# Kernel optimization log

Hardware: AMD Instinct MI355X
Metric: run time of the kernel (lower is better)

The kernel has to match this reference:

```python
import jax, jax.numpy as jnp
import numpy as np

N_NODES = 163840
N_EDGES = 2621440
F_IN = 64
F_HID = 64
SUBG = 20  # size_subgraph_samples
NEG_SLOPE = 0.2


def gat_conv(x, src, dst, W, a_src, a_dst, b):
    """PyG GATConv, heads=1, concat. src/dst already include self-loops."""
    n = x.shape[0]
    h = x @ W                               # [N, H]
    al_s = h @ a_src                        # [N]
    al_d = h @ a_dst                        # [N]
    e = jax.nn.leaky_relu(al_s[src] + al_d[dst], NEG_SLOPE)  # [E]
    # softmax over incoming edges of each dst node
    m = jax.ops.segment_max(e, dst, num_segments=n)
    ex = jnp.exp(e - m[dst])
    denom = jax.ops.segment_sum(ex, dst, num_segments=n)
    alpha = ex / (denom[dst] + 1e-16)
    msg = h[src] * alpha[:, None]           # [E, H]
    out = jax.ops.segment_sum(msg, dst, num_segments=n)
    return out + b


def setup_inputs() -> dict:
    key = jax.random.key(0)
    ks = jax.random.split(key, 12)
    s = 0.05
    return {
        "x": jax.random.normal(ks[0], (N_NODES, F_IN), jnp.float32),
        "edge_index": jax.random.randint(ks[1], (2, N_EDGES), 0, N_NODES, jnp.int64 if jax.config.jax_enable_x64 else jnp.int32),
        "W1": jax.random.normal(ks[2], (F_IN, F_HID), jnp.float32) * s,
        "a_src1": jax.random.normal(ks[3], (F_HID,), jnp.float32) * s,
        "a_dst1": jax.random.normal(ks[4], (F_HID,), jnp.float32) * s,
        "b1": jnp.zeros((F_HID,), jnp.float32),
        "W2": jax.random.normal(ks[5], (F_HID, F_HID), jnp.float32) * s,
        "a_src2": jax.random.normal(ks[6], (F_HID,), jnp.float32) * s,
        "a_dst2": jax.random.normal(ks[7], (F_HID,), jnp.float32) * s,
        "b2": jnp.zeros((F_HID,), jnp.float32),
        "W_out": jax.random.normal(ks[8], (F_HID * SUBG, 1), jnp.float32) * s,
        "b_out": jnp.zeros((1,), jnp.float32),
    }


def reference(x, edge_index, W1, a_src1, a_dst1, b1, W2, a_src2, a_dst2, b2, W_out, b_out):
    n = x.shape[0]
    loop = jnp.arange(n, dtype=edge_index.dtype)
    src = jnp.concatenate([edge_index[0], loop])  # add_self_loops=True
    dst = jnp.concatenate([edge_index[1], loop])
    h = gat_conv(x, src, dst, W1, a_src1, a_dst1, b1)
    h = jax.nn.relu(h)  # dropout is identity in eval mode
    h = gat_conv(h, src, dst, W2, a_src2, a_dst2, b2)
    h = jax.nn.relu(h)
    h = h.reshape(n // SUBG, F_HID * SUBG)
    return h @ W_out + b_out
```

## Files before the change

### kernel.cpp

```cpp
#include <hip/hip_runtime.h>
#include <math.h>

#define F 64
#define NPB 160
#define STAGE_CAP 6304

typedef __attribute__((ext_vector_type(8))) short bf16x8;
typedef __attribute__((ext_vector_type(4))) float f32x4;

__device__ inline unsigned short f2bf(float f) {
  unsigned int u = __float_as_uint(f);
  u += 0x7fffu + ((u >> 16) & 1u);
  return (unsigned short)(u >> 16);
}


__global__ __launch_bounds__(256) void k_bin_count(const int* __restrict__ edst, int* __restrict__ cntT,
                                                   int e, int ch, int nblk, int nb,
                                                   const float* __restrict__ W1, const float* __restrict__ W2,
                                                   uint4* __restrict__ wf) {
  __shared__ int h[1024];
  int k = blockIdx.x, tid = threadIdx.x;
  if (k == nblk) {
    for (int i = tid; i < 1024; i += 256) {
      int layer = i >> 9, rem = i & 511;
      int cb = rem >> 6, lane = rem & 63;
      int c = cb >> 1, kk = cb & 1;
      int l15 = lane & 15, quad = lane >> 4;
      const float* W = layer ? W2 : W1;
      unsigned short p[8];
      #pragma unroll
      for (int j = 0; j < 8; j++) {
        int kd = kk * 32 + quad * 8 + j;
        p[j] = f2bf(W[kd * F + c * 16 + l15]);
      }
      wf[i] = *(const uint4*)p;
    }
    return;
  }
  for (int i = tid; i < nb; i += 256) h[i] = 0;
  __syncthreads();
  int beg = k * ch, end = min(e, beg + ch);
  for (int i = beg + tid; i < end; i += 256) atomicAdd(&h[edst[i] / NPB], 1);
  __syncthreads();
  for (int b = tid; b < nb; b += 256) cntT[b * nblk + k] = h[b];
}

__global__ __launch_bounds__(256) void k_scan1(const int* __restrict__ counts, int* __restrict__ offs,
                                               int* __restrict__ bsums, int n) {
  int tid = threadIdx.x, lane = tid & 63, wv = tid >> 6;
  int i = blockIdx.x * 256 + tid;
  int v = (i < n) ? counts[i] : 0;
  int x = v;
  #pragma unroll
  for (int o = 1; o <= 32; o <<= 1) { int y = __shfl_up(x, o); if (lane >= o) x += y; }
  __shared__ int wsum[4];
  if (lane == 63) wsum[wv] = x;
  __syncthreads();
  int add = 0;
  for (int w = 0; w < wv; w++) add += wsum[w];
  int incl = x + add;
  if (i < n) offs[i] = incl - v;
  if (tid == 255) bsums[blockIdx.x] = incl;
}

__global__ __launch_bounds__(256) void k_scan2(int* __restrict__ bs, int nb,
                                               float* __restrict__ out, const float* __restrict__ bo, int ng) {
  __shared__ int wsum[4];
  __shared__ int carry_sh;
  int tid = threadIdx.x, lane = tid & 63, wv = tid >> 6;
  float b0 = bo[0];
  for (int i = tid; i < ng; i += 256) out[i] = b0;
  if (tid == 0) carry_sh = 0;
  __syncthreads();
  for (int base = 0; base < nb; base += 256) {
    int i = base + tid;
    int v = (i < nb) ? bs[i] : 0;
    int x = v;
    #pragma unroll
    for (int o = 1; o <= 32; o <<= 1) { int y = __shfl_up(x, o); if (lane >= o) x += y; }
    if (lane == 63) wsum[wv] = x;
    __syncthreads();
    int add = 0;
    for (int w = 0; w < wv; w++) add += wsum[w];
    int incl = x + add;
    int carry = carry_sh;
    if (i < nb) bs[i] = incl - v + carry;
    __syncthreads();
    if (tid == 255) carry_sh = carry + incl;
    __syncthreads();
  }
}

template<bool IN_BF16>
__device__ __forceinline__ void gemm_body(const void* __restrict__ in, const uint4* __restrict__ wf,
                                          const float* __restrict__ avs, const float* __restrict__ avd,
                                          unsigned short* __restrict__ hgb, float* __restrict__ als,
                                          float* __restrict__ ald, int n, int bid, int nbl) {
  int tid = threadIdx.x, lane = tid & 63, wv = tid >> 6;
  int l15 = lane & 15, quad = lane >> 4;
  bf16x8 bfr[4][2];
  #pragma unroll
  for (int cb = 0; cb < 8; cb++) {
    uint4 u = wf[cb * 64 + lane];
    bfr[cb >> 1][cb & 1] = *(const bf16x8*)&u;
  }
  float as_l[4], ad_l[4];
  #pragma unroll
  for (int c = 0; c < 4; c++) { as_l[c] = avs[c * 16 + l15]; ad_l[c] = avd[c * 16 + l15]; }

  int nchunks = n >> 6;
  for (int chunk = bid; chunk < nchunks; chunk += nbl) {
    int r0 = (chunk << 6) + (wv << 4);
    bf16x8 a0, a1;
    if constexpr (IN_BF16) {
      const uint4* row4 = (const uint4*)((const unsigned short*)in + (size_t)(r0 + l15) * F);
      uint4 u0 = row4[quad];
      uint4 u1 = row4[quad + 4];
      a0 = *(const bf16x8*)&u0;
      a1 = *(const bf16x8*)&u1;
    } else {
      const float4* xr = (const float4*)((const float*)in + (size_t)(r0 + l15) * F + quad * 8);
      float4 xa = xr[0], xb = xr[1];
      float4 xc = xr[8], xd = xr[9];
      a0[0] = (short)f2bf(xa.x); a0[1] = (short)f2bf(xa.y); a0[2] = (short)f2bf(xa.z); a0[3] = (short)f2bf(xa.w);
      a0[4] = (short)f2bf(xb.x); a0[5] = (short)f2bf(xb.y); a0[6] = (short)f2bf(xb.z); a0[7] = (short)f2bf(xb.w);
      a1[0] = (short)f2bf(xc.x); a1[1] = (short)f2bf(xc.y); a1[2] = (short)f2bf(xc.z); a1[3] = (short)f2bf(xc.w);
      a1[4] = (short)f2bf(xd.x); a1[5] = (short)f2bf(xd.y); a1[6] = (short)f2bf(xd.z); a1[7] = (short)f2bf(xd.w);
    }
    f32x4 cfr[4];
    #pragma unroll
    for (int c = 0; c < 4; c++) {
      cfr[c] = (f32x4){0.f, 0.f, 0.f, 0.f};
      cfr[c] = __builtin_amdgcn_mfma_f32_16x16x32_bf16(a0, bfr[c][0], cfr[c], 0, 0, 0);
      cfr[c] = __builtin_amdgcn_mfma_f32_16x16x32_bf16(a1, bfr[c][1], cfr[c], 0, 0, 0);
    }
    #pragma unroll
    for (int i = 0; i < 4; i++) {
      int row = r0 + quad * 4 + i;
      #pragma unroll
      for (int c = 0; c < 4; c++) hgb[(size_t)row * F + c * 16 + l15] = f2bf(cfr[c][i]);
      float ps = cfr[0][i] * as_l[0] + cfr[1][i] * as_l[1] + cfr[2][i] * as_l[2] + cfr[3][i] * as_l[3];
      float pd = cfr[0][i] * ad_l[0] + cfr[1][i] * ad_l[1] + cfr[2][i] * ad_l[2] + cfr[3][i] * ad_l[3];
      #pragma unroll
      for (int o = 1; o <= 8; o <<= 1) { ps += __shfl_xor(ps, o); pd += __shfl_xor(pd, o); }
      if (l15 == 0) { als[row] = ps; ald[row] = pd; }
    }
  }
}

__global__ __launch_bounds__(256) void k_scatter_gemm1(const int* __restrict__ esrc, const int* __restrict__ edst,
                                                       const int* __restrict__ posT, const int* __restrict__ bsums,
                                                       unsigned int* __restrict__ binned,
                                                       int e, int ch, int nblk, int nb,
                                                       const float* __restrict__ x, const uint4* __restrict__ wf,
                                                       const float* __restrict__ avs, const float* __restrict__ avd,
                                                       unsigned short* __restrict__ hgb, float* __restrict__ als,
                                                       float* __restrict__ ald, int n) {
  int k = blockIdx.x, tid = threadIdx.x;
  if (k < nblk) {
    __shared__ int cur[1024];
    for (int b = tid; b < nb; b += 256) {
      int idx = b * nblk + k;
      cur[b] = posT[idx] + bsums[idx >> 8];
    }
    __syncthreads();
    int beg = k * ch, end = min(e, beg + ch);
    for (int i = beg + tid; i < end; i += 256) {
      int d = edst[i];
      int b = d / NPB;
      unsigned int ld = (unsigned int)(d - b * NPB);
      int p = atomicAdd(&cur[b], 1);
      binned[p] = (unsigned int)esrc[i] | (ld << 24);
    }
    return;
  }
  gemm_body<false>(x, wf, avs, avd, hgb, als, ald, n, k - nblk, (int)gridDim.x - nblk);
}

__global__ __launch_bounds__(256) void k_gemm2(const unsigned short* __restrict__ in, const uint4* __restrict__ wf,
                                               const float* __restrict__ avs, const float* __restrict__ avd,
                                               unsigned short* __restrict__ hgb, float* __restrict__ als,
                                               float* __restrict__ ald, int n) {
  gemm_body<true>(in, wf, avs, avd, hgb, als, ald, n, blockIdx.x, gridDim.x);
}

__global__ __launch_bounds__(256) void k_bucket_csr(const unsigned int* __restrict__ binned,
                                                    const int* __restrict__ posT, const int* __restrict__ bsums,
                                                    int* __restrict__ ssrc, int* __restrict__ offs,
                                                    int n, int nblk, int nb, int e) {
  __shared__ int ncnt[NPB];
  __shared__ int noff[NPB];
  __shared__ int cur[NPB];
  __shared__ int sc[256];
  __shared__ int stage[STAGE_CAP];
  int b = blockIdx.x, tid = threadIdx.x;
  int node0 = b * NPB;
  int nn = min(NPB, n - node0);
  int i0 = b * nblk;
  int ebeg = posT[i0] + bsums[i0 >> 8];
  int eend;
  if (b == nb - 1) eend = e;
  else { int i1 = (b + 1) * nblk; eend = posT[i1] + bsums[i1 >> 8]; }
  int ecnt = eend - ebeg;
  for (int i = tid; i < NPB; i += 256) ncnt[i] = 0;
  __syncthreads();
  for (int i = tid; i < ecnt; i += 256) { unsigned int v = binned[ebeg + i]; atomicAdd(&ncnt[v >> 24], 1); }
  __syncthreads();
  int x = (tid < nn) ? ncnt[tid] + 1 : 0;
  sc[tid] = x;
  __syncthreads();
  #pragma unroll
  for (int o = 1; o < 256; o <<= 1) {
    int y = (tid >= o) ? sc[tid - o] : 0;
    __syncthreads();
    sc[tid] += y;
    __syncthreads();
  }
  if (tid < nn) noff[tid] = sc[tid] - x;
  __syncthreads();
  int tot = ecnt + nn;
  int outbase = ebeg + node0;
  bool staged = (tot <= STAGE_CAP);
  if (tid < nn) {
    cur[tid] = noff[tid] + 1;
    offs[node0 + tid] = outbase + noff[tid];
    if (staged) stage[noff[tid]] = node0 + tid;
    else        ssrc[outbase + noff[tid]] = node0 + tid;
  }
  __syncthreads();
  if (staged) {
    for (int i = tid; i < ecnt; i += 256) {
      unsigned int v = binned[ebeg + i];
      int p = atomicAdd(&cur[v >> 24], 1);
      stage[p] = (int)(v & 0xFFFFFFu);
    }
    __syncthreads();
    for (int i = tid; i < tot; i += 256) ssrc[outbase + i] = stage[i];
  } else {
    for (int i = tid; i < ecnt; i += 256) {
      unsigned int v = binned[ebeg + i];
      int p = atomicAdd(&cur[v >> 24], 1);
      ssrc[outbase + p] = (int)(v & 0xFFFFFFu);
    }
  }
  if (b == 0 && tid == 0) offs[n] = e + n;
}

template<int MODE>
__global__ __launch_bounds__(256) void k_spmm(const int* __restrict__ offs, const int* __restrict__ ssrc,
                                              const unsigned short* __restrict__ hgb,
                                              const float* __restrict__ als, const float* __restrict__ ald,
                                              const float* __restrict__ bias, const float* __restrict__ Wout,
                                              void* __restrict__ outp, int n) {
  int tid = threadIdx.x, lane = tid & 63, wv = tid >> 6;
  int g8 = lane >> 3, l8 = lane & 7;
  const uint4* hg4 = (const uint4*)hgb;
  float4 bl0 = ((const float4*)bias)[l8 * 2];
  float4 bl1 = ((const float4*)bias)[l8 * 2 + 1];

  __shared__ float gsl[3];
  if (MODE == 1 && tid < 3) gsl[tid] = 0.f;

  int node = (blockIdx.x * 4 + wv) * 8 + g8;
  int cnode = min(node, n - 1);
  bool nodeok = node < n;
  int beg = offs[cnode];
  int deg = nodeok ? (offs[cnode + 1] - beg) : 0;
  int degc = max(deg - 1, 0);
  float aldv = ald[cnode];

  int dm = deg;
  #pragma unroll
  for (int o = 8; o <= 32; o <<= 1) dm = max(dm, __shfl_xor(dm, o));

  float s = 0.f;
  float acc[8];
  #pragma unroll
  for (int k = 0; k < 8; k++) acc[k] = 0.f;

  #pragma unroll 2
  for (int j = 0; j < dm; j++) {
    int jj = min(j, degc);
    int src = ssrc[beg + jj];
    float t = als[src] + aldv;
    t = fmaxf(t, 0.2f * t);
    float ex = (j < deg) ? __expf(t) : 0.f;
    s += ex;
    uint4 u = hg4[(size_t)src * 8 + l8];
    acc[0] = fmaf(ex, __uint_as_float(u.x << 16), acc[0]);
    acc[1] = fmaf(ex, __uint_as_float(u.x & 0xffff0000u), acc[1]);
    acc[2] = fmaf(ex, __uint_as_float(u.y << 16), acc[2]);
    acc[3] = fmaf(ex, __uint_as_float(u.y & 0xffff0000u), acc[3]);
    acc[4] = fmaf(ex, __uint_as_float(u.z << 16), acc[4]);
    acc[5] = fmaf(ex, __uint_as_float(u.z & 0xffff0000u), acc[5]);
    acc[6] = fmaf(ex, __uint_as_float(u.w << 16), acc[6]);
    acc[7] = fmaf(ex, __uint_as_float(u.w & 0xffff0000u), acc[7]);
  }

  float iv = 1.f / (s + 1e-16f);
  float r[8];
  r[0] = fmaxf(fmaf(acc[0], iv, bl0.x), 0.f);
  r[1] = fmaxf(fmaf(acc[1], iv, bl0.y), 0.f);
  r[2] = fmaxf(fmaf(acc[2], iv, bl0.z), 0.f);
  r[3] = fmaxf(fmaf(acc[3], iv, bl0.w), 0.f);
  r[4] = fmaxf(fmaf(acc[4], iv, bl1.x), 0.f);
  r[5] = fmaxf(fmaf(acc[5], iv, bl1.y), 0.f);
  r[6] = fmaxf(fmaf(acc[6], iv, bl1.z), 0.f);
  r[7] = fmaxf(fmaf(acc[7], iv, bl1.w), 0.f);

  if constexpr (MODE == 0) {
    if (!nodeok) return;
    unsigned short p[8];
    #pragma unroll
    for (int k = 0; k < 8; k++) p[k] = f2bf(r[k]);
    ((uint4*)outp)[(size_t)node * 8 + l8] = *(const uint4*)p;
  } else {
    int node0 = blockIdx.x * 32;
    int grp0 = node0 / 20;
    int grp = cnode / 20, slot = cnode - grp * 20;
    const float* wr = Wout + slot * F + l8 * 8;
    float dot = 0.f;
    #pragma unroll
    for (int k = 0; k < 8; k++) dot = fmaf(r[k], wr[k], dot);
    #pragma unroll
    for (int o = 1; o <= 4; o <<= 1) dot += __shfl_xor(dot, o);
    __syncthreads();
    if (nodeok && l8 == 0) atomicAdd(&gsl[grp - grp0], dot);
    __syncthreads();
    if (tid < 3) {
      float v = gsl[tid];
      if (v != 0.f) atomicAdd((float*)outp + grp0 + tid, v);
    }
  }
}

extern "C" void kernel_launch(void* const* d_in, const int* in_sizes, int n_in,
                              void* d_out, int out_size, void* d_ws, size_t ws_size,
                              hipStream_t stream) {
  const float* x   = (const float*)d_in[0];
  const int*   ei  = (const int*)d_in[1];
  const float* W1  = (const float*)d_in[2];
  const float* as1 = (const float*)d_in[3];
  const float* ad1 = (const float*)d_in[4];
  const float* b1  = (const float*)d_in[5];
  const float* W2  = (const float*)d_in[6];
  const float* as2 = (const float*)d_in[7];
  const float* ad2 = (const float*)d_in[8];
  const float* b2  = (const float*)d_in[9];
  const float* Wo  = (const float*)d_in[10];
  const float* bo  = (const float*)d_in[11];
  float* out = (float*)d_out;

  const int N = in_sizes[0] / F;
  const int E = in_sizes[1] / 2;
  const int* esrc = ei;
  const int* edst = ei + E;

  size_t off = 0;
  auto alloc = [&](size_t bytes) -> void* {
    void* p = (char*)d_ws + off;
    off += (bytes + 255) & ~(size_t)255;
    return p;
  };
  float* A    = (float*)alloc((size_t)N * F * 4);
  unsigned short* hgb = (unsigned short*)alloc((size_t)N * F * 2);
  float* als  = (float*)alloc((size_t)N * 4);
  float* ald  = (float*)alloc((size_t)N * 4);
  int* offs   = (int*)alloc((size_t)(N + 1) * 4);
  int* bsums  = (int*)alloc(8192);
  int* ssrc   = (int*)alloc((size_t)(E + N) * 4);
  uint4* wf   = (uint4*)alloc(16384);
  (void)ws_size; (void)n_in; (void)out_size;

  const int NBLK = 256;
  const int NB = (N + NPB - 1) / NPB;
  const int CH = (E + NBLK - 1) / NBLK;
  const int FLAT = NB * NBLK;

  int* cntT = (int*)A;
  int* posT = (int*)((char*)A + ((size_t)FLAT * 4 + 1024));
  unsigned int* binned = (unsigned int*)((char*)A + (size_t)8 * 1024 * 1024);

  int gF = (FLAT + 255) / 256;
  int NG = N / 20;

  k_bin_count<<<NBLK + 1, 256, 0, stream>>>(edst, cntT, E, CH, NBLK, NB, W1, W2, wf);
  k_scan1<<<gF, 256, 0, stream>>>(cntT, posT, bsums, FLAT);
  k_scan2<<<1, 256, 0, stream>>>(bsums, gF, out, bo, NG);
  k_scatter_gemm1<<<NBLK + (N >> 6), 256, 0, stream>>>(esrc, edst, posT, bsums, binned, E, CH, NBLK, NB,
                                                       x, wf, as1, ad1, hgb, als, ald, N);
  k_bucket_csr<<<NB, 256, 0, stream>>>(binned, posT, bsums, ssrc, offs, N, NBLK, NB, E);

  int gSp = (N + 31) / 32;
  k_spmm<0><<<gSp, 256, 0, stream>>>(offs, ssrc, hgb, als, ald, b1, nullptr, A, N);
  k_gemm2<<<(N >> 6), 256, 0, stream>>>((const unsigned short*)A, wf + 512, as2, ad2, hgb, als, ald, N);
  k_spmm<1><<<gSp, 256, 0, stream>>>(offs, ssrc, hgb, als, ald, b2, Wo, out, N);
}
```

Baseline: 309.8 us.

## Sort edges locally per chunk in one pass and gather bucket runs from chunks

```diff
diff --git a/kernel.cpp b/kernel.cpp
--- a/kernel.cpp
+++ b/kernel.cpp
@@ -3,7 +3,6 @@
 
 #define F 64
 #define NPB 160
-#define STAGE_CAP 6304
 
 typedef __attribute__((ext_vector_type(8))) short bf16x8;
 typedef __attribute__((ext_vector_type(4))) float f32x4;
@@ -14,96 +13,32 @@
   return (unsigned short)(u >> 16);
 }
 
-
-__global__ __launch_bounds__(256) void k_bin_count(const int* __restrict__ edst, int* __restrict__ cntT,
-                                                   int e, int ch, int nblk, int nb,
-                                                   const float* __restrict__ W1, const float* __restrict__ W2,
-                                                   uint4* __restrict__ wf) {
-  __shared__ int h[1024];
-  int k = blockIdx.x, tid = threadIdx.x;
-  if (k == nblk) {
-    for (int i = tid; i < 1024; i += 256) {
-      int layer = i >> 9, rem = i & 511;
-      int cb = rem >> 6, lane = rem & 63;
-      int c = cb >> 1, kk = cb & 1;
-      int l15 = lane & 15, quad = lane >> 4;
-      const float* W = layer ? W2 : W1;
-      unsigned short p[8];
-      #pragma unroll
-      for (int j = 0; j < 8; j++) {
-        int kd = kk * 32 + quad * 8 + j;
-        p[j] = f2bf(W[kd * F + c * 16 + l15]);
-      }
-      wf[i] = *(const uint4*)p;
-    }
-    return;
-  }
-  for (int i = tid; i < nb; i += 256) h[i] = 0;
-  __syncthreads();
-  int beg = k * ch, end = min(e, beg + ch);
-  for (int i = beg + tid; i < end; i += 256) atomicAdd(&h[edst[i] / NPB], 1);
-  __syncthreads();
-  for (int b = tid; b < nb; b += 256) cntT[b * nblk + k] = h[b];
-}
-
-__global__ __launch_bounds__(256) void k_scan1(const int* __restrict__ counts, int* __restrict__ offs,
-                                               int* __restrict__ bsums, int n) {
-  int tid = threadIdx.x, lane = tid & 63, wv = tid >> 6;
-  int i = blockIdx.x * 256 + tid;
-  int v = (i < n) ? counts[i] : 0;
-  int x = v;
-  #pragma unroll
-  for (int o = 1; o <= 32; o <<= 1) { int y = __shfl_up(x, o); if (lane >= o) x += y; }
-  __shared__ int wsum[4];
-  if (lane == 63) wsum[wv] = x;
-  __syncthreads();
-  int add = 0;
-  for (int w = 0; w < wv; w++) add += wsum[w];
-  int incl = x + add;
-  if (i < n) offs[i] = incl - v;
-  if (tid == 255) bsums[blockIdx.x] = incl;
-}
-
-__global__ __launch_bounds__(256) void k_scan2(int* __restrict__ bs, int nb,
-                                               float* __restrict__ out, const float* __restrict__ bo, int ng) {
-  __shared__ int wsum[4];
-  __shared__ int carry_sh;
-  int tid = threadIdx.x, lane = tid & 63, wv = tid >> 6;
-  float b0 = bo[0];
-  for (int i = tid; i < ng; i += 256) out[i] = b0;
-  if (tid == 0) carry_sh = 0;
-  __syncthreads();
-  for (int base = 0; base < nb; base += 256) {
-    int i = base + tid;
-    int v = (i < nb) ? bs[i] : 0;
-    int x = v;
-    #pragma unroll
-    for (int o = 1; o <= 32; o <<= 1) { int y = __shfl_up(x, o); if (lane >= o) x += y; }
-    if (lane == 63) wsum[wv] = x;
-    __syncthreads();
-    int add = 0;
-    for (int w = 0; w < wv; w++) add += wsum[w];
-    int incl = x + add;
-    int carry = carry_sh;
-    if (i < nb) bs[i] = incl - v + carry;
-    __syncthreads();
-    if (tid == 255) carry_sh = carry + incl;
-    __syncthreads();
-  }
-}
-
-template<bool IN_BF16>
-__device__ __forceinline__ void gemm_body(const void* __restrict__ in, const uint4* __restrict__ wf,
+template<bool IN_BF16, bool PACKED>
+__device__ __forceinline__ void gemm_body(const void* __restrict__ in, const void* __restrict__ Wsrc,
                                           const float* __restrict__ avs, const float* __restrict__ avd,
                                           unsigned short* __restrict__ hgb, float* __restrict__ als,
                                           float* __restrict__ ald, int n, int bid, int nbl) {
   int tid = threadIdx.x, lane = tid & 63, wv = tid >> 6;
   int l15 = lane & 15, quad = lane >> 4;
   bf16x8 bfr[4][2];
-  #pragma unroll
-  for (int cb = 0; cb < 8; cb++) {
-    uint4 u = wf[cb * 64 + lane];
-    bfr[cb >> 1][cb & 1] = *(const bf16x8*)&u;
+  if constexpr (PACKED) {
+    const uint4* wf = (const uint4*)Wsrc;
+    #pragma unroll
+    for (int cb = 0; cb < 8; cb++) {
+      uint4 u = wf[cb * 64 + lane];
+      bfr[cb >> 1][cb & 1] = *(const bf16x8*)&u;
+    }
+  } else {
+    const float* W = (const float*)Wsrc;
+    #pragma unroll
+    for (int c = 0; c < 4; c++)
+      #pragma unroll
+      for (int kk = 0; kk < 2; kk++)
+        #pragma unroll
+        for (int j = 0; j < 8; j++) {
+          int kd = kk * 32 + quad * 8 + j;
+          bfr[c][kk][j] = (short)f2bf(W[kd * F + c * 16 + l15]);
+        }
   }
   float as_l[4], ad_l[4];
   #pragma unroll
@@ -149,63 +84,144 @@
   }
 }
 
-__global__ __launch_bounds__(256) void k_scatter_gemm1(const int* __restrict__ esrc, const int* __restrict__ edst,
-                                                       const int* __restrict__ posT, const int* __restrict__ bsums,
-                                                       unsigned int* __restrict__ binned,
-                                                       int e, int ch, int nblk, int nb,
-                                                       const float* __restrict__ x, const uint4* __restrict__ wf,
-                                                       const float* __restrict__ avs, const float* __restrict__ avd,
-                                                       unsigned short* __restrict__ hgb, float* __restrict__ als,
-                                                       float* __restrict__ ald, int n) {
+__global__ __launch_bounds__(256) void k_sort_gemm1(const int* __restrict__ esrc, const int* __restrict__ edst,
+                                                    int* __restrict__ cntT, int* __restrict__ lstart,
+                                                    unsigned int* __restrict__ binned,
+                                                    int e, int ch, int nblk, int nb,
+                                                    const float* __restrict__ x, const float* __restrict__ W1,
+                                                    const float* __restrict__ avs, const float* __restrict__ avd,
+                                                    unsigned short* __restrict__ hgb, float* __restrict__ als,
+                                                    float* __restrict__ ald, int n) {
   int k = blockIdx.x, tid = threadIdx.x;
-  if (k < nblk) {
-    __shared__ int cur[1024];
-    for (int b = tid; b < nb; b += 256) {
-      int idx = b * nblk + k;
-      cur[b] = posT[idx] + bsums[idx >> 8];
-    }
-    __syncthreads();
-    int beg = k * ch, end = min(e, beg + ch);
-    for (int i = beg + tid; i < end; i += 256) {
-      int d = edst[i];
-      int b = d / NPB;
-      unsigned int ld = (unsigned int)(d - b * NPB);
-      int p = atomicAdd(&cur[b], 1);
-      binned[p] = (unsigned int)esrc[i] | (ld << 24);
-    }
+  if (k >= nblk) {
+    gemm_body<false, false>(x, W1, avs, avd, hgb, als, ald, n, k - nblk, (int)gridDim.x - nblk);
     return;
   }
-  gemm_body<false>(x, wf, avs, avd, hgb, als, ald, n, k - nblk, (int)gridDim.x - nblk);
-}
-
-__global__ __launch_bounds__(256) void k_gemm2(const unsigned short* __restrict__ in, const uint4* __restrict__ wf,
-                                               const float* __restrict__ avs, const float* __restrict__ avd,
-                                               unsigned short* __restrict__ hgb, float* __restrict__ als,
-                                               float* __restrict__ ald, int n) {
-  gemm_body<true>(in, wf, avs, avd, hgb, als, ald, n, blockIdx.x, gridDim.x);
+  __shared__ int h[1024];
+  __shared__ int cur[1024];
+  __shared__ int sc[256];
+  for (int i = tid; i < 1024; i += 256) h[i] = 0;
+  __syncthreads();
+  int beg = k * ch, end = min(e, beg + ch);
+  for (int i = beg + tid; i < end; i += 256) atomicAdd(&h[edst[i] / NPB], 1);
+  __syncthreads();
+  int s0 = h[tid * 4], s1 = h[tid * 4 + 1], s2 = h[tid * 4 + 2], s3 = h[tid * 4 + 3];
+  int tot = s0 + s1 + s2 + s3;
+  sc[tid] = tot;
+  __syncthreads();
+  #pragma unroll
+  for (int o = 1; o < 256; o <<= 1) {
+    int y = (tid >= o) ? sc[tid - o] : 0;
+    __syncthreads();
+    sc[tid] += y;
+    __syncthreads();
+  }
+  int base = sc[tid] - tot;
+  int e0 = base, e1 = base + s0, e2 = e1 + s1, e3 = e2 + s2;
+  cur[tid * 4] = beg + e0; cur[tid * 4 + 1] = beg + e1;
+  cur[tid * 4 + 2] = beg + e2; cur[tid * 4 + 3] = beg + e3;
+  int4 ls = make_int4(e0, e1, e2, e3);
+  *(int4*)&lstart[k * 1024 + tid * 4] = ls;
+  if (tid * 4 + 0 < nb) cntT[(tid * 4 + 0) * nblk + k] = s0;
+  if (tid * 4 + 1 < nb) cntT[(tid * 4 + 1) * nblk + k] = s1;
+  if (tid * 4 + 2 < nb) cntT[(tid * 4 + 2) * nblk + k] = s2;
+  if (tid * 4 + 3 < nb) cntT[(tid * 4 + 3) * nblk + k] = s3;
+  __syncthreads();
+  for (int i = beg + tid; i < end; i += 256) {
+    int d = edst[i];
+    int b = d / NPB;
+    unsigned int ld = (unsigned int)(d - b * NPB);
+    int p = atomicAdd(&cur[b], 1);
+    binned[p] = (unsigned int)esrc[i] | (ld << 24);
+  }
+}
+
+__global__ __launch_bounds__(256) void k_scan1(const int* __restrict__ counts, int* __restrict__ offs,
+                                               int* __restrict__ bsums, int n,
+                                               const float* __restrict__ W2, uint4* __restrict__ wf) {
+  int tid = threadIdx.x;
+  if (blockIdx.x == gridDim.x - 1) {
+    for (int i = tid; i < 512; i += 256) {
+      int cb = i >> 6, lane = i & 63;
+      int c = cb >> 1, kk = cb & 1;
+      int l15 = lane & 15, quad = lane >> 4;
+      unsigned short p[8];
+      #pragma unroll
+      for (int j = 0; j < 8; j++) {
+        int kd = kk * 32 + quad * 8 + j;
+        p[j] = f2bf(W2[kd * F + c * 16 + l15]);
+      }
+      wf[i] = *(const uint4*)p;
+    }
+    return;
+  }
+  int lane = tid & 63, wv = tid >> 6;
+  int i = blockIdx.x * 256 + tid;
+  int v = (i < n) ? counts[i] : 0;
+  int x = v;
+  #pragma unroll
+  for (int o = 1; o <= 32; o <<= 1) { int y = __shfl_up(x, o); if (lane >= o) x += y; }
+  __shared__ int wsum[4];
+  if (lane == 63) wsum[wv] = x;
+  __syncthreads();
+  int add = 0;
+  for (int w = 0; w < wv; w++) add += wsum[w];
+  int incl = x + add;
+  if (i < n) offs[i] = incl - v;
+  if (tid == 255) bsums[blockIdx.x] = incl;
+}
+
+__global__ __launch_bounds__(256) void k_scan2(int* __restrict__ bs, int nb,
+                                               float* __restrict__ out, const float* __restrict__ bo, int ng) {
+  __shared__ int wsum[4];
+  __shared__ int carry_sh;
+  int tid = threadIdx.x, lane = tid & 63, wv = tid >> 6;
+  float b0 = bo[0];
+  for (int i = tid; i < ng; i += 256) out[i] = b0;
+  if (tid == 0) carry_sh = 0;
+  __syncthreads();
+  for (int base = 0; base < nb; base += 256) {
+    int i = base + tid;
+    int v = (i < nb) ? bs[i] : 0;
+    int x = v;
+    #pragma unroll
+    for (int o = 1; o <= 32; o <<= 1) { int y = __shfl_up(x, o); if (lane >= o) x += y; }
+    if (lane == 63) wsum[wv] = x;
+    __syncthreads();
+    int add = 0;
+    for (int w = 0; w < wv; w++) add += wsum[w];
+    int incl = x + add;
+    int carry = carry_sh;
+    if (i < nb) bs[i] = incl - v + carry;
+    __syncthreads();
+    if (tid == 255) carry_sh = carry + incl;
+    __syncthreads();
+  }
 }
 
 __global__ __launch_bounds__(256) void k_bucket_csr(const unsigned int* __restrict__ binned,
                                                     const int* __restrict__ posT, const int* __restrict__ bsums,
+                                                    const int* __restrict__ cntT, const int* __restrict__ lstart,
                                                     int* __restrict__ ssrc, int* __restrict__ offs,
-                                                    int n, int nblk, int nb, int e) {
+                                                    int n, int nblk, int nb, int e, int ch) {
   __shared__ int ncnt[NPB];
-  __shared__ int noff[NPB];
   __shared__ int cur[NPB];
   __shared__ int sc[256];
-  __shared__ int stage[STAGE_CAP];
+  __shared__ int runbase[256];
+  __shared__ int runlen[256];
   int b = blockIdx.x, tid = threadIdx.x;
   int node0 = b * NPB;
   int nn = min(NPB, n - node0);
   int i0 = b * nblk;
   int ebeg = posT[i0] + bsums[i0 >> 8];
-  int eend;
-  if (b == nb - 1) eend = e;
-  else { int i1 = (b + 1) * nblk; eend = posT[i1] + bsums[i1 >> 8]; }
-  int ecnt = eend - ebeg;
+  runlen[tid] = cntT[i0 + tid];
+  runbase[tid] = tid * ch + lstart[tid * 1024 + b];
   for (int i = tid; i < NPB; i += 256) ncnt[i] = 0;
   __syncthreads();
-  for (int i = tid; i < ecnt; i += 256) { unsigned int v = binned[ebeg + i]; atomicAdd(&ncnt[v >> 24], 1); }
+  {
+    int len = runlen[tid], base = runbase[tid];
+    for (int j = 0; j < len; j++) { unsigned int v = binned[base + j]; atomicAdd(&ncnt[v >> 24], 1); }
+  }
   __syncthreads();
   int x = (tid < nn) ? ncnt[tid] + 1 : 0;
   sc[tid] = x;
@@ -217,34 +233,30 @@
     sc[tid] += y;
     __syncthreads();
   }
-  if (tid < nn) noff[tid] = sc[tid] - x;
-  __syncthreads();
-  int tot = ecnt + nn;
+  int noff = sc[tid] - x;
   int outbase = ebeg + node0;
-  bool staged = (tot <= STAGE_CAP);
   if (tid < nn) {
-    cur[tid] = noff[tid] + 1;
-    offs[node0 + tid] = outbase + noff[tid];
-    if (staged) stage[noff[tid]] = node0 + tid;
-    else        ssrc[outbase + noff[tid]] = node0 + tid;
-  }
-  __syncthreads();
-  if (staged) {
-    for (int i = tid; i < ecnt; i += 256) {
-      unsigned int v = binned[ebeg + i];
-      int p = atomicAdd(&cur[v >> 24], 1);
-      stage[p] = (int)(v & 0xFFFFFFu);
-    }
-    __syncthreads();
-    for (int i = tid; i < tot; i += 256) ssrc[outbase + i] = stage[i];
-  } else {
-    for (int i = tid; i < ecnt; i += 256) {
-      unsigned int v = binned[ebeg + i];
+    cur[tid] = noff + 1;
+    offs[node0 + tid] = outbase + noff;
+    ssrc[outbase + noff] = node0 + tid;
+  }
+  __syncthreads();
+  {
+    int len = runlen[tid], base = runbase[tid];
+    for (int j = 0; j < len; j++) {
+      unsigned int v = binned[base + j];
       int p = atomicAdd(&cur[v >> 24], 1);
       ssrc[outbase + p] = (int)(v & 0xFFFFFFu);
     }
   }
   if (b == 0 && tid == 0) offs[n] = e + n;
+}
+
+__global__ __launch_bounds__(256) void k_gemm2(const unsigned short* __restrict__ in, const uint4* __restrict__ wf,
+                                               const float* __restrict__ avs, const float* __restrict__ avd,
+                                               unsigned short* __restrict__ hgb, float* __restrict__ als,
+                                               float* __restrict__ ald, int n) {
+  gemm_body<true, true>(in, wf, avs, avd, hgb, als, ald, n, blockIdx.x, gridDim.x);
 }
 
 template<int MODE>
@@ -370,7 +382,7 @@
   int* offs   = (int*)alloc((size_t)(N + 1) * 4);
   int* bsums  = (int*)alloc(8192);
   int* ssrc   = (int*)alloc((size_t)(E + N) * 4);
-  uint4* wf   = (uint4*)alloc(16384);
+  uint4* wf   = (uint4*)alloc(8192);
   (void)ws_size; (void)n_in; (void)out_size;
 
   const int NBLK = 256;
@@ -378,22 +390,22 @@
   const int CH = (E + NBLK - 1) / NBLK;
   const int FLAT = NB * NBLK;
 
-  int* cntT = (int*)A;
-  int* posT = (int*)((char*)A + ((size_t)FLAT * 4 + 1024));
-  unsigned int* binned = (unsigned int*)((char*)A + (size_t)8 * 1024 * 1024);
+  int* cntT            = (int*)A;
+  int* posT            = (int*)((char*)A + (size_t)2 * 1024 * 1024);
+  int* lstart          = (int*)((char*)A + (size_t)4 * 1024 * 1024);
+  unsigned int* binned = (unsigned int*)((char*)A + (size_t)6 * 1024 * 1024);
 
   int gF = (FLAT + 255) / 256;
   int NG = N / 20;
 
-  k_bin_count<<<NBLK + 1, 256, 0, stream>>>(edst, cntT, E, CH, NBLK, NB, W1, W2, wf);
-  k_scan1<<<gF, 256, 0, stream>>>(cntT, posT, bsums, FLAT);
+  k_sort_gemm1<<<NBLK + (N >> 6), 256, 0, stream>>>(esrc, edst, cntT, lstart, binned, E, CH, NBLK, NB,
+                                                    x, W1, as1, ad1, hgb, als, ald, N);
+  k_scan1<<<gF + 1, 256, 0, stream>>>(cntT, posT, bsums, FLAT, W2, wf);
   k_scan2<<<1, 256, 0, stream>>>(bsums, gF, out, bo, NG);
-  k_scatter_gemm1<<<NBLK + (N >> 6), 256, 0, stream>>>(esrc, edst, posT, bsums, binned, E, CH, NBLK, NB,
-                                                       x, wf, as1, ad1, hgb, als, ald, N);
-  k_bucket_csr<<<NB, 256, 0, stream>>>(binned, posT, bsums, ssrc, offs, N, NBLK, NB, E);
+  k_bucket_csr<<<NB, 256, 0, stream>>>(binned, posT, bsums, cntT, lstart, ssrc, offs, N, NBLK, NB, E, CH);
 
   int gSp = (N + 31) / 32;
   k_spmm<0><<<gSp, 256, 0, stream>>>(offs, ssrc, hgb, als, ald, b1, nullptr, A, N);
-  k_gemm2<<<(N >> 6), 256, 0, stream>>>((const unsigned short*)A, wf + 512, as2, ad2, hgb, als, ald, N);
+  k_gemm2<<<(N >> 6), 256, 0, stream>>>((const unsigned short*)A, wf, as2, ad2, hgb, als, ald, N);
   k_spmm<1><<<gSp, 256, 0, stream>>>(offs, ssrc, hgb, als, ald, b2, Wo, out, N);
 }
```

Measured after the change: 316.8 us. 2.3% more time.
